# Kernel tuning notes

Measured on AMD Instinct MI355X. Metric: run time of the kernel, lower is better.

The kernel has to match this reference:

```python
import jax, jax.numpy as jnp
import numpy as np

D_MODEL = 1024
H = 16
D_K = D_MODEL // H


def setup_inputs() -> dict:
    key = jax.random.key(0)
    ks = jax.random.split(key, 12)
    B, S = 4, 2048
    scale = 1.0 / np.sqrt(D_MODEL)
    inp = {
        "q": jax.random.normal(ks[0], (B, S, D_MODEL), jnp.float32),
        "k": jax.random.normal(ks[1], (B, S, D_MODEL), jnp.float32),
        "v": jax.random.normal(ks[2], (B, S, D_MODEL), jnp.float32),
        "mask": jnp.ones((1, 1, S, S), dtype=bool),
        "Wq": jax.random.normal(ks[3], (D_MODEL, D_MODEL), jnp.float32) * scale,
        "bq": jax.random.normal(ks[4], (D_MODEL,), jnp.float32) * scale,
        "Wk": jax.random.normal(ks[5], (D_MODEL, D_MODEL), jnp.float32) * scale,
        "bk": jax.random.normal(ks[6], (D_MODEL,), jnp.float32) * scale,
        "Wv": jax.random.normal(ks[7], (D_MODEL, D_MODEL), jnp.float32) * scale,
        "bv": jax.random.normal(ks[8], (D_MODEL,), jnp.float32) * scale,
        "Wo": jax.random.normal(ks[9], (D_MODEL, D_MODEL), jnp.float32) * scale,
        "bo": jax.random.normal(ks[10], (D_MODEL,), jnp.float32) * scale,
    }
    return inp


def reference(q, k, v, mask, Wq, bq, Wk, bk, Wv, bv, Wo, bo):
    B, S, D = q.shape
    # QKV projections (torch Linear: x @ W.T + b), split into heads [B,H,S,d_k]
    Q = (q @ Wq.T + bq).reshape(B, S, H, D_K).transpose(0, 2, 1, 3)
    K = (k @ Wk.T + bk).reshape(B, S, H, D_K).transpose(0, 2, 1, 3)
    V = (v @ Wv.T + bv).reshape(B, S, H, D_K).transpose(0, 2, 1, 3)
    # scaled dot-product attention; NOTE: original's masked_fill result is
    # discarded (non-inplace), so the mask has no effect — faithfully ignored.
    scores = jnp.einsum("bhqd,bhkd->bhqk", Q, K) / jnp.sqrt(jnp.float32(D_K))
    attn = jax.nn.softmax(scores, axis=-1)  # dropout = identity (eval mode)
    x = jnp.einsum("bhqk,bhkd->bhqd", attn, V)
    x = x.transpose(0, 2, 1, 3).reshape(B, S, D)
    return x @ Wo.T + bo
```

## Files before the change

kernel.cpp:

```cpp
#include <hip/hip_runtime.h>
#include <stdint.h>

#define Bb 4
#define Ss 2048
#define Dd 1024
#define Hh 16
#define DKk 64
#define Mm (Bb * Ss)

typedef __attribute__((ext_vector_type(4))) float f32x4;
typedef __attribute__((ext_vector_type(16))) float f32x16;
typedef __attribute__((ext_vector_type(4))) float f4v;
typedef __attribute__((ext_vector_type(8))) unsigned short us8;
typedef __attribute__((ext_vector_type(4))) unsigned short us4;
typedef __attribute__((ext_vector_type(8))) __bf16 bf16x8;

__device__ __forceinline__ unsigned short bfbits(__bf16 x) {
  union { __bf16 b; unsigned short u; } v; v.b = x; return v.u;
}
__device__ __forceinline__ uint32_t packbf(float lo, float hi) {
  union { __bf16 b[2]; uint32_t u; } v;
  v.b[0] = (__bf16)lo; v.b[1] = (__bf16)hi;
  return v.u;
}
__device__ __forceinline__ void plswap(uint32_t& a, uint32_t& b) {
  asm("v_permlane32_swap_b32 %0, %1" : "+v"(a), "+v"(b));
}
__device__ __forceinline__ void gl16(const unsigned short* g, unsigned short* l) {
  __builtin_amdgcn_global_load_lds(
      (__attribute__((address_space(1))) void*)(g),
      (__attribute__((address_space(3))) void*)(l), 16, 0, 0);
}

__global__ __launch_bounds__(256)
void split_hilo(const float* __restrict__ x, unsigned short* __restrict__ hi,
                unsigned short* __restrict__ lo, int n4) {
  int i = blockIdx.x * 256 + threadIdx.x;
  if (i >= n4) return;
  f4v v = *(const f4v*)(x + (size_t)i * 4);
  us4 h, l;
#pragma unroll
  for (int j = 0; j < 4; ++j) {
    __bf16 hb = (__bf16)v[j];
    h[j] = bfbits(hb);
    l[j] = bfbits((__bf16)(v[j] - (float)hb));
  }
  *(us4*)(hi + (size_t)i * 4) = h;
  *(us4*)(lo + (size_t)i * 4) = l;
}

__global__ __launch_bounds__(256)
void cvt3_bf16(const float* __restrict__ x0, unsigned short* __restrict__ o0,
               const float* __restrict__ x1, unsigned short* __restrict__ o1,
               const float* __restrict__ x2, unsigned short* __restrict__ o2,
               int n4) {
  int i = blockIdx.x * 256 + threadIdx.x;
  if (i >= n4) return;
  const float* x = (blockIdx.y == 0) ? x0 : (blockIdx.y == 1) ? x1 : x2;
  unsigned short* o = (blockIdx.y == 0) ? o0 : (blockIdx.y == 1) ? o1 : o2;
  f4v v = *(const f4v*)(x + (size_t)i * 4);
  us4 h;
#pragma unroll
  for (int j = 0; j < 4; ++j) h[j] = bfbits((__bf16)v[j]);
  *(us4*)(o + (size_t)i * 4) = h;
}

template <bool BSPLIT, bool OUT_BF16>
__global__ __launch_bounds__(256)
void gemm_bt(const unsigned short* __restrict__ A,
             const unsigned short* __restrict__ Bh, const unsigned short* __restrict__ Bl,
             const float* __restrict__ bias, void* __restrict__ outp,
             int Kdim, int Ndim, float scale) {
  __shared__ unsigned short Ath[128 * 64];
  __shared__ unsigned short Bth[128 * 64];
  __shared__ unsigned short Btl[BSPLIT ? 128 * 64 : 8];

  const int tid = threadIdx.x;
  const int wave = tid >> 6, lane = tid & 63, g = lane >> 4, ln = lane & 15;
  const int wr = wave >> 1, wc = wave & 1;
  int dd = blockIdx.x;
  int orig = (dd & 7) * 64 + (dd >> 3);
  const int bm = (orig >> 3) * 128;
  const int bn = (orig & 7) * 128;

  const int srow = lane >> 3;
  const int schunk = (lane & 7) ^ srow;

  f32x4 acc[4][4] = {};

  for (int k0 = 0; k0 < Kdim; k0 += 64) {
    __syncthreads();
#pragma unroll
    for (int ii = 0; ii < 4; ++ii) {
      const int rA = wave * 32 + ii * 8;
      gl16(&A [(size_t)(bm + rA + srow) * Kdim + k0 + schunk * 8], &Ath[rA * 64]);
      gl16(&Bh[(size_t)(bn + rA + srow) * Kdim + k0 + schunk * 8], &Bth[rA * 64]);
      if constexpr (BSPLIT) {
        gl16(&Bl[(size_t)(bn + rA + srow) * Kdim + k0 + schunk * 8], &Btl[rA * 64]);
      }
    }
    __syncthreads();

#pragma unroll
    for (int ko = 0; ko < 2; ++ko) {
      bf16x8 ah[4], bh[4], bl[4];
#pragma unroll
      for (int i = 0; i < 4; ++i) {
        const int ra = wr * 64 + i * 16 + ln;
        const int rb = wc * 64 + i * 16 + ln;
        ah[i] = *(const bf16x8*)&Ath[ra * 64 + ((ko * 4 + g) ^ (ra & 7)) * 8];
        bh[i] = *(const bf16x8*)&Bth[rb * 64 + ((ko * 4 + g) ^ (rb & 7)) * 8];
        if constexpr (BSPLIT) {
          bl[i] = *(const bf16x8*)&Btl[rb * 64 + ((ko * 4 + g) ^ (rb & 7)) * 8];
        }
      }
#pragma unroll
      for (int i = 0; i < 4; ++i)
#pragma unroll
        for (int j = 0; j < 4; ++j) {
          acc[i][j] = __builtin_amdgcn_mfma_f32_16x16x32_bf16(ah[i], bh[j], acc[i][j], 0, 0, 0);
          if constexpr (BSPLIT) {
            acc[i][j] = __builtin_amdgcn_mfma_f32_16x16x32_bf16(ah[i], bl[j], acc[i][j], 0, 0, 0);
          }
        }
    }
  }

  float bvals[4];
#pragma unroll
  for (int j = 0; j < 4; ++j) bvals[j] = bias[bn + wc * 64 + j * 16 + ln];

#pragma unroll
  for (int i = 0; i < 4; ++i) {
    int row0 = bm + wr * 64 + i * 16 + g * 4;
#pragma unroll
    for (int j = 0; j < 4; ++j) {
      int col = bn + wc * 64 + j * 16 + ln;
#pragma unroll
      for (int r = 0; r < 4; ++r) {
        float vv = (acc[i][j][r] + bvals[j]) * scale;
        if constexpr (OUT_BF16) {
          ((unsigned short*)outp)[(size_t)(row0 + r) * Ndim + col] = bfbits((__bf16)vv);
        } else {
          ((float*)outp)[(size_t)(row0 + r) * Ndim + col] = vv;
        }
      }
    }
  }
}

__global__ __launch_bounds__(256)
void gemm_vT(const unsigned short* __restrict__ A,
             const unsigned short* __restrict__ Bh, const unsigned short* __restrict__ Bl,
             const float* __restrict__ bias, unsigned short* __restrict__ VT,
             int Kdim, int Ndim) {
  __shared__ unsigned short S[3 * 128 * 64];
  unsigned short* Ath = S;
  unsigned short* Bth = S + 8192;
  unsigned short* Btl = S + 16384;

  const int tid = threadIdx.x;
  const int wave = tid >> 6, lane = tid & 63, g = lane >> 4, ln = lane & 15;
  const int wr = wave >> 1, wc = wave & 1;
  int dd = blockIdx.x;
  int orig = (dd & 7) * 64 + (dd >> 3);
  const int bm = (orig >> 3) * 128;
  const int bn = (orig & 7) * 128;

  const int srow = lane >> 3;
  const int schunk = (lane & 7) ^ srow;

  f32x4 acc[4][4] = {};

  for (int k0 = 0; k0 < Kdim; k0 += 64) {
    __syncthreads();
#pragma unroll
    for (int ii = 0; ii < 4; ++ii) {
      const int rA = wave * 32 + ii * 8;
      gl16(&A [(size_t)(bm + rA + srow) * Kdim + k0 + schunk * 8], &Ath[rA * 64]);
      gl16(&Bh[(size_t)(bn + rA + srow) * Kdim + k0 + schunk * 8], &Bth[rA * 64]);
      gl16(&Bl[(size_t)(bn + rA + srow) * Kdim + k0 + schunk * 8], &Btl[rA * 64]);
    }
    __syncthreads();

#pragma unroll
    for (int ko = 0; ko < 2; ++ko) {
      bf16x8 ah[4], bh[4], bl[4];
#pragma unroll
      for (int i = 0; i < 4; ++i) {
        const int ra = wr * 64 + i * 16 + ln;
        const int rb = wc * 64 + i * 16 + ln;
        ah[i] = *(const bf16x8*)&Ath[ra * 64 + ((ko * 4 + g) ^ (ra & 7)) * 8];
        bh[i] = *(const bf16x8*)&Bth[rb * 64 + ((ko * 4 + g) ^ (rb & 7)) * 8];
        bl[i] = *(const bf16x8*)&Btl[rb * 64 + ((ko * 4 + g) ^ (rb & 7)) * 8];
      }
#pragma unroll
      for (int i = 0; i < 4; ++i)
#pragma unroll
        for (int j = 0; j < 4; ++j) {
          acc[i][j] = __builtin_amdgcn_mfma_f32_16x16x32_bf16(ah[i], bh[j], acc[i][j], 0, 0, 0);
          acc[i][j] = __builtin_amdgcn_mfma_f32_16x16x32_bf16(ah[i], bl[j], acc[i][j], 0, 0, 0);
        }
    }
  }

  float bvals[4];
#pragma unroll
  for (int j = 0; j < 4; ++j) bvals[j] = bias[bn + wc * 64 + j * 16 + ln];

  __syncthreads();
#pragma unroll
  for (int i = 0; i < 4; ++i) {
    int sl0 = wr * 64 + i * 16 + g * 4;
#pragma unroll
    for (int j = 0; j < 4; ++j) {
      int dl = wc * 64 + j * 16 + ln;
      us4 w;
#pragma unroll
      for (int r = 0; r < 4; ++r) w[r] = bfbits((__bf16)(acc[i][j][r] + bvals[j]));
      *(us4*)&S[dl * 132 + sl0] = w;
    }
  }
  __syncthreads();

  const int bb = bm >> 11, s0g = bm & 2047;
#pragma unroll
  for (int it = 0; it < 8; ++it) {
    int u = it * 256 + tid;
    int dl = u >> 4, sc = (u & 15) * 8;
    us8 o = *(const us8*)&S[dl * 132 + sc];
    *(us8*)&VT[((size_t)bb * Dd + bn + dl) * Ss + s0g + sc] = o;
  }
}

__global__ __launch_bounds__(256, 4)
void attn_fused(const unsigned short* __restrict__ Qb, const unsigned short* __restrict__ Kb,
                const unsigned short* __restrict__ VT, unsigned short* __restrict__ xb) {
  __shared__ unsigned short Ks[2][64 * 64];
  __shared__ unsigned short Vs[2][64 * 64];

  const int tid = threadIdx.x, wave = tid >> 6, lane = tid & 63;
  const int lq = lane & 31, hi = lane >> 5;
  const int swzc = (lane & 7) ^ ((lane >> 3) & 7);

  int dd = blockIdx.x;
  int orig = (dd & 7) * 128 + (dd >> 3);
  const int bh = orig >> 4, qb = orig & 15;
  const int q0 = qb * 128;
  const int b = bh >> 4, h = bh & 15;

  const size_t rowBase = (size_t)b * Ss * Dd + (size_t)h * DKk;
  const size_t vtBase  = ((size_t)b * Dd + h * DKk) * Ss;

  bf16x8 qf[4];
  {
    const unsigned short* qrow =
        Qb + rowBase + (size_t)(q0 + wave * 32 + lq) * Dd + 8 * hi;
#pragma unroll
    for (int c = 0; c < 4; ++c) qf[c] = *(const bf16x8*)(qrow + 16 * c);
  }

  bf16x8 ones;
#pragma unroll
  for (int j = 0; j < 8; ++j) ones[j] = (__bf16)1.0f;

  f32x16 accO[2] = {};
  f32x16 acc_l = {};

  const int i0 = wave * 2;
  auto stage = [&](int t, int nb) {
#pragma unroll
    for (int ii = 0; ii < 2; ++ii) {
      const int i = i0 + ii;
      const int rr = i * 8 + (lane >> 3);
      gl16(&Kb[rowBase + (size_t)(t * 64 + rr) * Dd + swzc * 8], &Ks[nb][i * 512]);
      gl16(&VT[vtBase + (size_t)rr * Ss + t * 64 + swzc * 8], &Vs[nb][i * 512]);
    }
  };

  stage(0, 0);

  for (int t = 0; t < 32; ++t) {
    const int cur = t & 1;
    __syncthreads();
    if (t + 1 < 32) stage(t + 1, 1 - cur);

    uint32_t pf[4][4];
#pragma unroll
    for (int s = 0; s < 2; ++s) {
      f32x16 z = {};
#pragma unroll
      for (int c = 0; c < 4; ++c) {
        bf16x8 kf = *(const bf16x8*)
            &Ks[cur][(s * 32 + lq) * 64 + ((2 * c + hi) ^ (lq & 7)) * 8];
        z = __builtin_amdgcn_mfma_f32_32x32x16_bf16(kf, qf[c], z, 0, 0, 0);
      }
      uint32_t w[8];
#pragma unroll
      for (int i = 0; i < 8; ++i) {
        float e0 = __builtin_amdgcn_exp2f(z[2 * i]);
        float e1 = __builtin_amdgcn_exp2f(z[2 * i + 1]);
        w[i] = packbf(e0, e1);
      }
#pragma unroll
      for (int mm = 0; mm < 2; ++mm) {
        uint32_t a0 = w[4 * mm + 0], b0 = w[4 * mm + 2];
        uint32_t a1 = w[4 * mm + 1], b1 = w[4 * mm + 3];
        plswap(a0, b0);
        plswap(a1, b1);
        pf[2 * s + mm][0] = a0;
        pf[2 * s + mm][1] = a1;
        pf[2 * s + mm][2] = b0;
        pf[2 * s + mm][3] = b1;
      }
    }

    __builtin_amdgcn_s_setprio(1);
#pragma unroll
    for (int m = 0; m < 4; ++m) {
      bf16x8 pa = *(const bf16x8*)&pf[m][0];
      acc_l = __builtin_amdgcn_mfma_f32_32x32x16_bf16(pa, ones, acc_l, 0, 0, 0);
#pragma unroll
      for (int ds = 0; ds < 2; ++ds) {
        bf16x8 bv = *(const bf16x8*)
            &Vs[cur][(ds * 32 + lq) * 64 + ((2 * m + hi) ^ (lq & 7)) * 8];
        accO[ds] = __builtin_amdgcn_mfma_f32_32x32x16_bf16(pa, bv, accO[ds], 0, 0, 0);
      }
    }
    __builtin_amdgcn_s_setprio(0);
  }

#pragma unroll
  for (int ds = 0; ds < 2; ++ds)
#pragma unroll
    for (int r = 0; r < 16; ++r) {
      int q = (r & 3) + 8 * (r >> 2) + 4 * hi;
      size_t row = (size_t)b * Ss + q0 + wave * 32 + q;
      xb[row * Dd + h * DKk + ds * 32 + lq] =
          bfbits((__bf16)(accO[ds][r] / acc_l[r]));
    }
}

extern "C" void kernel_launch(void* const* d_in, const int* in_sizes, int n_in,
                              void* d_out, int out_size, void* d_ws, size_t ws_size,
                              hipStream_t stream) {
  const float* q  = (const float*)d_in[0];
  const float* k  = (const float*)d_in[1];
  const float* v  = (const float*)d_in[2];
  const float* Wq = (const float*)d_in[4];
  const float* bq = (const float*)d_in[5];
  const float* Wk = (const float*)d_in[6];
  const float* bk = (const float*)d_in[7];
  const float* Wv = (const float*)d_in[8];
  const float* bv = (const float*)d_in[9];
  const float* Wo = (const float*)d_in[10];
  const float* bo = (const float*)d_in[11];

  char* ws = (char*)d_ws;
  const size_t SZT = (size_t)Mm * Dd * 2;
  const size_t SZW = (size_t)Dd * Dd * 2;
  const size_t need = 5 * SZT + 8 * SZW;
  if (ws_size < need) return;

  unsigned short* ab_q = (unsigned short*)(ws + 0 * SZT);
  unsigned short* ab_k = (unsigned short*)(ws + 1 * SZT);
  unsigned short* ab_v = (unsigned short*)(ws + 2 * SZT);
  char* wbase = ws + 3 * SZT;
  unsigned short* Wqh = (unsigned short*)(wbase + 0 * SZW);
  unsigned short* Wkh = (unsigned short*)(wbase + 1 * SZW);
  unsigned short* Wvh = (unsigned short*)(wbase + 2 * SZW);
  unsigned short* Wvl = (unsigned short*)(wbase + 3 * SZW);
  unsigned short* Woh = (unsigned short*)(wbase + 4 * SZW);
  char* base2 = wbase + 8 * SZW;
  unsigned short* Qb = (unsigned short*)(base2 + 0 * SZT);
  unsigned short* Kb = (unsigned short*)(base2 + 1 * SZT);
  unsigned short* VTp = ab_q;
  unsigned short* xbp = ab_k;

  const int n4t = Mm * Dd / 4;
  const int n4w = Dd * Dd / 4;
  const float QSCALE = 0.125f * 1.44269504f;

  cvt3_bf16<<<dim3(n4w / 256, 3), 256, 0, stream>>>(Wq, Wqh, Wk, Wkh, Wo, Woh, n4w);
  split_hilo<<<n4w / 256, 256, 0, stream>>>(Wv, Wvh, Wvl, n4w);

  cvt3_bf16<<<dim3(n4t / 256, 3), 256, 0, stream>>>(q, ab_q, k, ab_k, v, ab_v, n4t);

  gemm_bt<false, true><<<512, 256, 0, stream>>>(ab_q, Wqh, Wqh, bq, Qb, Dd, Dd, QSCALE);
  gemm_bt<false, true><<<512, 256, 0, stream>>>(ab_k, Wkh, Wkh, bk, Kb, Dd, Dd, 1.0f);
  gemm_vT<<<512, 256, 0, stream>>>(ab_v, Wvh, Wvl, bv, VTp, Dd, Dd);

  attn_fused<<<1024, 256, 0, stream>>>(Qb, Kb, VTp, xbp);

  gemm_bt<false, false><<<512, 256, 0, stream>>>(xbp, Woh, Woh, bo, d_out, Dd, Dd, 1.0f);
}
```

Before: 237.0 us.

## Fuse Q/K/V projections into one launch and drop the Wv hi/lo split

Result: faster. 215.6 us (-9.0%).

```diff
diff --git a/kernel.cpp b/kernel.cpp
--- a/kernel.cpp
+++ b/kernel.cpp
@@ -33,20 +33,21 @@
 }
 
 __global__ __launch_bounds__(256)
-void split_hilo(const float* __restrict__ x, unsigned short* __restrict__ hi,
-                unsigned short* __restrict__ lo, int n4) {
+void wprep(const float* __restrict__ Wq, unsigned short* __restrict__ oq,
+           const float* __restrict__ Wk, unsigned short* __restrict__ ok,
+           const float* __restrict__ Wv, unsigned short* __restrict__ ov,
+           const float* __restrict__ Wo, unsigned short* __restrict__ oo,
+           int n4) {
   int i = blockIdx.x * 256 + threadIdx.x;
   if (i >= n4) return;
+  int w = blockIdx.y;
+  const float* x = (w == 0) ? Wq : (w == 1) ? Wk : (w == 2) ? Wv : Wo;
+  unsigned short* o = (w == 0) ? oq : (w == 1) ? ok : (w == 2) ? ov : oo;
   f4v v = *(const f4v*)(x + (size_t)i * 4);
-  us4 h, l;
-#pragma unroll
-  for (int j = 0; j < 4; ++j) {
-    __bf16 hb = (__bf16)v[j];
-    h[j] = bfbits(hb);
-    l[j] = bfbits((__bf16)(v[j] - (float)hb));
-  }
-  *(us4*)(hi + (size_t)i * 4) = h;
-  *(us4*)(lo + (size_t)i * 4) = l;
+  us4 h;
+#pragma unroll
+  for (int j = 0; j < 4; ++j) h[j] = bfbits((__bf16)v[j]);
+  *(us4*)(o + (size_t)i * 4) = h;
 }
 
 __global__ __launch_bounds__(256)
@@ -65,6 +66,119 @@
   *(us4*)(o + (size_t)i * 4) = h;
 }
 
+__global__ __launch_bounds__(256)
+void gemm_qkv(const unsigned short* __restrict__ Aq, const unsigned short* __restrict__ Ak,
+              const unsigned short* __restrict__ Av,
+              const unsigned short* __restrict__ Wqh, const unsigned short* __restrict__ Wkh,
+              const unsigned short* __restrict__ Wvh,
+              const float* __restrict__ bq, const float* __restrict__ bk,
+              const float* __restrict__ bv,
+              unsigned short* __restrict__ Qb, unsigned short* __restrict__ Kb,
+              unsigned short* __restrict__ VT, float qscale) {
+  __shared__ unsigned short S[2 * 128 * 64];
+  unsigned short* Ath = S;
+  unsigned short* Bth = S + 8192;
+
+  const int tid = threadIdx.x;
+  const int wave = tid >> 6, lane = tid & 63, g = lane >> 4, ln = lane & 15;
+  const int wr = wave >> 1, wc = wave & 1;
+  int dd = blockIdx.x;
+  const int slot = dd >> 3;
+  const int op = slot >> 6;
+  const int orig = (dd & 7) * 64 + (slot & 63);
+  const int bm = (orig >> 3) * 128;
+  const int bn = (orig & 7) * 128;
+
+  const unsigned short* A  = (op == 0) ? Aq : (op == 1) ? Ak : Av;
+  const unsigned short* Bh = (op == 0) ? Wqh : (op == 1) ? Wkh : Wvh;
+  const float* bias        = (op == 0) ? bq : (op == 1) ? bk : bv;
+  const float scale        = (op == 0) ? qscale : 1.0f;
+
+  const int srow = lane >> 3;
+  const int schunk = (lane & 7) ^ srow;
+
+  f32x4 acc[4][4] = {};
+
+  for (int k0 = 0; k0 < Dd; k0 += 64) {
+    __syncthreads();
+#pragma unroll
+    for (int ii = 0; ii < 4; ++ii) {
+      const int rA = wave * 32 + ii * 8;
+      gl16(&A [(size_t)(bm + rA + srow) * Dd + k0 + schunk * 8], &Ath[rA * 64]);
+      gl16(&Bh[(size_t)(bn + rA + srow) * Dd + k0 + schunk * 8], &Bth[rA * 64]);
+    }
+    __syncthreads();
+
+#pragma unroll
+    for (int ko = 0; ko < 2; ++ko) {
+      bf16x8 ah[4], bh[4];
+#pragma unroll
+      for (int i = 0; i < 4; ++i) {
+        const int ra = wr * 64 + i * 16 + ln;
+        const int rb = wc * 64 + i * 16 + ln;
+        ah[i] = *(const bf16x8*)&Ath[ra * 64 + ((ko * 4 + g) ^ (ra & 7)) * 8];
+        bh[i] = *(const bf16x8*)&Bth[rb * 64 + ((ko * 4 + g) ^ (rb & 7)) * 8];
+      }
+#pragma unroll
+      for (int i = 0; i < 4; ++i)
+#pragma unroll
+        for (int j = 0; j < 4; ++j)
+          acc[i][j] = __builtin_amdgcn_mfma_f32_16x16x32_bf16(ah[i], bh[j], acc[i][j], 0, 0, 0);
+    }
+  }
+
+  float bvals[4];
+#pragma unroll
+  for (int j = 0; j < 4; ++j) bvals[j] = bias[bn + wc * 64 + j * 16 + ln];
+
+  if (op < 2) {
+    unsigned short* outp = op ? Kb : Qb;
+#pragma unroll
+    for (int i = 0; i < 4; ++i) {
+      int row0 = bm + wr * 64 + i * 16 + g * 4;
+#pragma unroll
+      for (int j = 0; j < 4; ++j) {
+        int col = bn + wc * 64 + j * 16 + ln;
+#pragma unroll
+        for (int r = 0; r < 4; ++r) {
+          float vv = (acc[i][j][r] + bvals[j]) * scale;
+          outp[(size_t)(row0 + r) * Dd + col] = bfbits((__bf16)vv);
+        }
+      }
+    }
+    return;
+  }
+
+  const int bb = bm >> 11, s0g = bm & 2047;
+  __syncthreads();
+#pragma unroll
+  for (int p = 0; p < 2; ++p) {
+    if (wr == p) {
+#pragma unroll
+      for (int i = 0; i < 4; ++i) {
+        int sl0 = i * 16 + g * 4;
+#pragma unroll
+        for (int j = 0; j < 4; ++j) {
+          int dl = wc * 64 + j * 16 + ln;
+          us4 w;
+#pragma unroll
+          for (int r = 0; r < 4; ++r) w[r] = bfbits((__bf16)(acc[i][j][r] + bvals[j]));
+          *(us4*)&S[dl * 68 + sl0] = w;
+        }
+      }
+    }
+    __syncthreads();
+#pragma unroll
+    for (int it = 0; it < 4; ++it) {
+      int u = it * 256 + tid;
+      int dl = u >> 3, sc = (u & 7) * 8;
+      us8 o = *(const us8*)&S[dl * 68 + sc];
+      *(us8*)&VT[((size_t)bb * Dd + bn + dl) * Ss + s0g + p * 64 + sc] = o;
+    }
+    __syncthreads();
+  }
+}
+
 template <bool BSPLIT, bool OUT_BF16>
 __global__ __launch_bounds__(256)
 void gemm_bt(const unsigned short* __restrict__ A,
@@ -146,90 +260,6 @@
         }
       }
     }
-  }
-}
-
-__global__ __launch_bounds__(256)
-void gemm_vT(const unsigned short* __restrict__ A,
-             const unsigned short* __restrict__ Bh, const unsigned short* __restrict__ Bl,
-             const float* __restrict__ bias, unsigned short* __restrict__ VT,
-             int Kdim, int Ndim) {
-  __shared__ unsigned short S[3 * 128 * 64];
-  unsigned short* Ath = S;
-  unsigned short* Bth = S + 8192;
-  unsigned short* Btl = S + 16384;
-
-  const int tid = threadIdx.x;
-  const int wave = tid >> 6, lane = tid & 63, g = lane >> 4, ln = lane & 15;
-  const int wr = wave >> 1, wc = wave & 1;
-  int dd = blockIdx.x;
-  int orig = (dd & 7) * 64 + (dd >> 3);
-  const int bm = (orig >> 3) * 128;
-  const int bn = (orig & 7) * 128;
-
-  const int srow = lane >> 3;
-  const int schunk = (lane & 7) ^ srow;
-
-  f32x4 acc[4][4] = {};
-
-  for (int k0 = 0; k0 < Kdim; k0 += 64) {
-    __syncthreads();
-#pragma unroll
-    for (int ii = 0; ii < 4; ++ii) {
-      const int rA = wave * 32 + ii * 8;
-      gl16(&A [(size_t)(bm + rA + srow) * Kdim + k0 + schunk * 8], &Ath[rA * 64]);
-      gl16(&Bh[(size_t)(bn + rA + srow) * Kdim + k0 + schunk * 8], &Bth[rA * 64]);
-      gl16(&Bl[(size_t)(bn + rA + srow) * Kdim + k0 + schunk * 8], &Btl[rA * 64]);
-    }
-    __syncthreads();
-
-#pragma unroll
-    for (int ko = 0; ko < 2; ++ko) {
-      bf16x8 ah[4], bh[4], bl[4];
-#pragma unroll
-      for (int i = 0; i < 4; ++i) {
-        const int ra = wr * 64 + i * 16 + ln;
-        const int rb = wc * 64 + i * 16 + ln;
-        ah[i] = *(const bf16x8*)&Ath[ra * 64 + ((ko * 4 + g) ^ (ra & 7)) * 8];
-        bh[i] = *(const bf16x8*)&Bth[rb * 64 + ((ko * 4 + g) ^ (rb & 7)) * 8];
-        bl[i] = *(const bf16x8*)&Btl[rb * 64 + ((ko * 4 + g) ^ (rb & 7)) * 8];
-      }
-#pragma unroll
-      for (int i = 0; i < 4; ++i)
-#pragma unroll
-        for (int j = 0; j < 4; ++j) {
-          acc[i][j] = __builtin_amdgcn_mfma_f32_16x16x32_bf16(ah[i], bh[j], acc[i][j], 0, 0, 0);
-          acc[i][j] = __builtin_amdgcn_mfma_f32_16x16x32_bf16(ah[i], bl[j], acc[i][j], 0, 0, 0);
-        }
-    }
-  }
-
-  float bvals[4];
-#pragma unroll
-  for (int j = 0; j < 4; ++j) bvals[j] = bias[bn + wc * 64 + j * 16 + ln];
-
-  __syncthreads();
-#pragma unroll
-  for (int i = 0; i < 4; ++i) {
-    int sl0 = wr * 64 + i * 16 + g * 4;
-#pragma unroll
-    for (int j = 0; j < 4; ++j) {
-      int dl = wc * 64 + j * 16 + ln;
-      us4 w;
-#pragma unroll
-      for (int r = 0; r < 4; ++r) w[r] = bfbits((__bf16)(acc[i][j][r] + bvals[j]));
-      *(us4*)&S[dl * 132 + sl0] = w;
-    }
-  }
-  __syncthreads();
-
-  const int bb = bm >> 11, s0g = bm & 2047;
-#pragma unroll
-  for (int it = 0; it < 8; ++it) {
-    int u = it * 256 + tid;
-    int dl = u >> 4, sc = (u & 15) * 8;
-    us8 o = *(const us8*)&S[dl * 132 + sc];
-    *(us8*)&VT[((size_t)bb * Dd + bn + dl) * Ss + s0g + sc] = o;
   }
 }
 
@@ -369,8 +399,7 @@
   unsigned short* Wqh = (unsigned short*)(wbase + 0 * SZW);
   unsigned short* Wkh = (unsigned short*)(wbase + 1 * SZW);
   unsigned short* Wvh = (unsigned short*)(wbase + 2 * SZW);
-  unsigned short* Wvl = (unsigned short*)(wbase + 3 * SZW);
-  unsigned short* Woh = (unsigned short*)(wbase + 4 * SZW);
+  unsigned short* Woh = (unsigned short*)(wbase + 3 * SZW);
   char* base2 = wbase + 8 * SZW;
   unsigned short* Qb = (unsigned short*)(base2 + 0 * SZT);
   unsigned short* Kb = (unsigned short*)(base2 + 1 * SZT);
@@ -381,16 +410,16 @@
   const int n4w = Dd * Dd / 4;
   const float QSCALE = 0.125f * 1.44269504f;
 
-  cvt3_bf16<<<dim3(n4w / 256, 3), 256, 0, stream>>>(Wq, Wqh, Wk, Wkh, Wo, Woh, n4w);
-  split_hilo<<<n4w / 256, 256, 0, stream>>>(Wv, Wvh, Wvl, n4w);
+  wprep<<<dim3(n4w / 256, 4), 256, 0, stream>>>(Wq, Wqh, Wk, Wkh, Wv, Wvh, Wo, Woh, n4w);
 
   cvt3_bf16<<<dim3(n4t / 256, 3), 256, 0, stream>>>(q, ab_q, k, ab_k, v, ab_v, n4t);
 
-  gemm_bt<false, true><<<512, 256, 0, stream>>>(ab_q, Wqh, Wqh, bq, Qb, Dd, Dd, QSCALE);
-  gemm_bt<false, true><<<512, 256, 0, stream>>>(ab_k, Wkh, Wkh, bk, Kb, Dd, Dd, 1.0f);
-  gemm_vT<<<512, 256, 0, stream>>>(ab_v, Wvh, Wvl, bv, VTp, Dd, Dd);
-
-  attn_fused<<<1024, 256, 0, stream>>>(Qb, Kb, VTp, xbp);
+  (void)VTp;
+  unsigned short* VTs = (unsigned short*)(base2 + 2 * SZT);
+  gemm_qkv<<<1536, 256, 0, stream>>>(ab_q, ab_k, ab_v, Wqh, Wkh, Wvh,
+                                     bq, bk, bv, Qb, Kb, VTs, QSCALE);
+
+  attn_fused<<<1024, 256, 0, stream>>>(Qb, Kb, VTs, xbp);
 
   gemm_bt<false, false><<<512, 256, 0, stream>>>(xbp, Woh, Woh, bo, d_out, Dd, Dd, 1.0f);
 }
```
